# Performance work log

Hardware: AMD Instinct MI355X
Metric: run time of the kernel (lower is better)

## Reference

```python
import jax, jax.numpy as jnp
import numpy as np


def setup_inputs() -> dict:
    key = jax.random.key(0)
    k1, k2 = jax.random.split(key)
    B, D, H, W = 16, 256, 32, 32
    K = 2048
    z = jax.random.normal(k1, (B, D, H, W), dtype=jnp.float32)
    # EmbeddingEMA init: uniform(-1/K, 1/K); plain randn scaled works as a stand-in param
    codebook = jax.random.uniform(k2, (K, D), dtype=jnp.float32,
                                  minval=-1.0 / K, maxval=1.0 / K)
    return {"z": z, "codebook": codebook}


def reference(z, codebook):
    # z: (B, D, H, W) -> (B, H, W, D) -> (n, D)   [normalize == 'none' path]
    B, D, H, W = z.shape
    z_flat = jnp.transpose(z, (0, 2, 3, 1)).reshape(-1, D)          # (n, D)
    z_norm = z_flat
    codebook_norm = codebook                                         # (K, D)

    # squared L2 distance: ||z||^2 + ||c||^2 - 2 z c^T   -> (n, K)
    distance = (jnp.sum(z_norm * z_norm, axis=1, keepdims=True)
                + jnp.sum(codebook_norm * codebook_norm, axis=1)
                - 2.0 * jnp.matmul(z_norm, codebook_norm.T))

    vq_indices = jnp.argmin(distance, axis=1)                        # (n,)
    z_q = codebook_norm[vq_indices]                                  # gather (n, D)

    # straight-through estimator (standard VQ forward output)
    z_q_st = z_norm + jax.lax.stop_gradient(z_q - z_norm)
    out = z_q_st.reshape(B, H, W, D).transpose(0, 3, 1, 2)           # (B, D, H, W)
    return out
```

## Files before the change

kernel.cpp:

```cpp
#include <hip/hip_runtime.h>
#include <stdint.h>


#define D_    256
#define K_    2048
#define HW_   1024
#define MT    64
#define NT    256
#define KT    16
#define SPLIT 4
#define KS    (K_ / SPLIT)
#define CST   256
#define BUFSZ (KT * MT + KT * CST)
#define NPH   ((KS / NT) * KT)
#define NPIX  16384

typedef float v2f __attribute__((ext_vector_type(2)));

__device__ __forceinline__ void gload16(const float* g, float* l) {
    auto* gp = reinterpret_cast<const __attribute__((address_space(1))) uint32_t*>(
        reinterpret_cast<uintptr_t>(g));
    auto* lp = reinterpret_cast<__attribute__((address_space(3))) uint32_t*>(
        reinterpret_cast<uintptr_t>(l));
    __builtin_amdgcn_global_load_lds(gp, lp, 16, 0, 0);
}

__device__ __forceinline__ float pw8(const float r[8]) {
    float t01 = __fadd_rn(r[0], r[1]);
    float t23 = __fadd_rn(r[2], r[3]);
    float L   = __fadd_rn(t01, t23);
    float t45 = __fadd_rn(r[4], r[5]);
    float t67 = __fadd_rn(r[6], r[7]);
    float R   = __fadd_rn(t45, t67);
    return __fadd_rn(L, R);
}

__global__ __launch_bounds__(256) void prep_k(const float* __restrict__ z,
                                              const float* __restrict__ cb,
                                              float* __restrict__ ct,
                                              float* __restrict__ An,
                                              float* __restrict__ Bn) {
    __shared__ float t[64][65];
    int tid = threadIdx.x;
    int bx  = blockIdx.x;
    if (bx < 128) {
        int k0 = (bx & 31) << 6;
        int d0 = (bx >> 5) << 6;
        #pragma unroll
        for (int it = 0; it < 4; ++it) {
            int u  = (it << 8) + tid;
            int kk = u >> 4;
            int dd = (u & 15) << 2;
            float4 v = *reinterpret_cast<const float4*>(
                cb + (size_t)(k0 + kk) * D_ + d0 + dd);
            t[kk][dd + 0] = v.x; t[kk][dd + 1] = v.y;
            t[kk][dd + 2] = v.z; t[kk][dd + 3] = v.w;
        }
        __syncthreads();
        #pragma unroll
        for (int it = 0; it < 4; ++it) {
            int u  = (it << 8) + tid;
            int dd = u >> 4;
            int kk = (u & 15) << 2;
            float4 o;
            o.x = t[kk + 0][dd]; o.y = t[kk + 1][dd];
            o.z = t[kk + 2][dd]; o.w = t[kk + 3][dd];
            *reinterpret_cast<float4*>(ct + (size_t)(d0 + dd) * K_ + k0 + kk) = o;
        }
    } else if (bx < 136) {
        int row = (bx - 128) * 256 + tid;
        const float4* p = reinterpret_cast<const float4*>(cb + (size_t)row * D_);
        float rA[8], rB[8];
        #pragma unroll
        for (int j = 0; j < 8; ++j) { rA[j] = 0.f; rB[j] = 0.f; }
        #pragma unroll
        for (int q = 0; q < 64; ++q) {
            float4 v = p[q];
            float pv[4] = {__fmul_rn(v.x, v.x), __fmul_rn(v.y, v.y),
                           __fmul_rn(v.z, v.z), __fmul_rn(v.w, v.w)};
            if (q < 32) {
                #pragma unroll
                for (int l = 0; l < 4; ++l)
                    rA[(4 * q + l) & 7] = __fadd_rn(rA[(4 * q + l) & 7], pv[l]);
            } else {
                #pragma unroll
                for (int l = 0; l < 4; ++l)
                    rB[(4 * q + l) & 7] = __fadd_rn(rB[(4 * q + l) & 7], pv[l]);
            }
        }
        Bn[row] = __fadd_rn(pw8(rA), pw8(rB));
    } else {
        int blk = bx - 136;
        int b   = blk >> 2;
        int hw0 = (blk & 3) << 8;
        const float* zb = z + (size_t)b * (D_ * HW_) + hw0 + tid;
        float rA[8], rB[8];
        #pragma unroll
        for (int j = 0; j < 8; ++j) { rA[j] = 0.f; rB[j] = 0.f; }
        #pragma unroll 8
        for (int d = 0; d < 128; ++d) {
            float v = zb[(size_t)d * HW_];
            rA[d & 7] = __fadd_rn(rA[d & 7], __fmul_rn(v, v));
        }
        #pragma unroll 8
        for (int d = 128; d < 256; ++d) {
            float v = zb[(size_t)d * HW_];
            rB[d & 7] = __fadd_rn(rB[d & 7], __fmul_rn(v, v));
        }
        An[(size_t)b * HW_ + hw0 + tid] = __fadd_rn(pw8(rA), pw8(rB));
    }
}

__global__ __launch_bounds__(256, 2) void vq_k(const float* __restrict__ z,
                                               const float* __restrict__ ct,
                                               const float* __restrict__ An,
                                               const float* __restrict__ Bn,
                                               float* __restrict__ pscore,
                                               int* __restrict__ pidx) {
    __shared__ float smem[2 * BUFSZ];
    float* rs = smem;
    int*   ri = (int*)(smem + MT * 33);

    const int tid  = threadIdx.x;
    const int lane = tid & 63;
    const int w    = tid >> 6;
    const int tn   = (tid & 7) | (w << 3);
    const int tm   = (tid >> 3) & 7;
    const int blk  = blockIdx.x;
    const int p    = blk / SPLIT;
    const int s    = blk % SPLIT;
    const int b      = p >> 4;
    const int hwbase = (p & 15) << 6;
    const float* zbase = z + (size_t)b * (D_ * HW_) + hwbase;
    const float* ctS   = ct + s * KS;

    const float* zsrc = zbase + (size_t)((w << 2) + (lane >> 4)) * HW_
                              + ((lane & 15) << 2);

    float bs[8]; int bi[8];
    #pragma unroll
    for (int i = 0; i < 8; ++i) { bs[i] = 1e30f; bi[i] = 0; }
    v2f acc[8][4];
    #pragma unroll
    for (int i = 0; i < 8; ++i)
        #pragma unroll
        for (int jp = 0; jp < 4; ++jp) acc[i][jp] = (v2f){0.f, 0.f};

    #define STAGE(ph)                                                         \
        do {                                                                  \
            int buf_ = (ph) & 1, kc_ = (ph) & 15, nc_ = (ph) >> 4;            \
            float* zb_ = smem + buf_ * BUFSZ;                                 \
            float* cb_ = zb_ + KT * MT;                                       \
            gload16(zsrc + (size_t)kc_ * (KT * HW_), zb_ + (w << 2) * MT);    \
            _Pragma("unroll")                                                 \
            for (int r = 0; r < 4; ++r) {                                     \
                int row = (w << 2) + r;                                       \
                gload16(ctS + (size_t)((kc_ << 4) + row) * K_ + nc_ * NT      \
                            + (lane << 2),                                    \
                        cb_ + row * CST);                                     \
            }                                                                 \
        } while (0)

    STAGE(0);

    for (int ph = 0; ph < NPH; ++ph) {
        __syncthreads();
        if (ph < NPH - 1) STAGE(ph + 1);
        const float* zb_ = smem + (ph & 1) * BUFSZ;
        const float* cb_ = zb_ + KT * MT;
        #pragma unroll
        for (int d = 0; d < KT; ++d) {
            const float* zr = zb_ + d * MT + (tm << 3);
            float4 a0 = *reinterpret_cast<const float4*>(zr);
            float4 a1 = *reinterpret_cast<const float4*>(zr + 4);
            const float* cr = cb_ + d * CST + (tn << 3);
            float4 b0 = *reinterpret_cast<const float4*>(cr);
            float4 b1 = *reinterpret_cast<const float4*>(cr + 4);
            v2f bp0 = {b0.x, b0.y}, bp1 = {b0.z, b0.w};
            v2f bp2 = {b1.x, b1.y}, bp3 = {b1.z, b1.w};
            float az[8] = {a0.x, a0.y, a0.z, a0.w, a1.x, a1.y, a1.z, a1.w};
            #pragma unroll
            for (int i = 0; i < 8; ++i) {
                v2f ai = {az[i], az[i]};
                acc[i][0] = __builtin_elementwise_fma(ai, bp0, acc[i][0]);
                acc[i][1] = __builtin_elementwise_fma(ai, bp1, acc[i][1]);
                acc[i][2] = __builtin_elementwise_fma(ai, bp2, acc[i][2]);
                acc[i][3] = __builtin_elementwise_fma(ai, bp3, acc[i][3]);
            }
        }
        if ((ph & 15) == 15) {
            int nc = ph >> 4;
            #pragma unroll
            for (int j = 0; j < 8; ++j) {
                int ng = s * KS + nc * NT + (tn << 3) + j;
                float bn = Bn[ng];
                #pragma unroll
                for (int i = 0; i < 8; ++i) {
                    float an = An[(size_t)b * HW_ + hwbase + (tm << 3) + i];
                    float sc = __fsub_rn(__fadd_rn(an, bn),
                                         __fmul_rn(2.0f, acc[i][j >> 1][j & 1]));
                    if (sc < bs[i]) { bs[i] = sc; bi[i] = ng; }
                }
            }
            #pragma unroll
            for (int i = 0; i < 8; ++i) {
                acc[i][0] = (v2f){0.f, 0.f}; acc[i][1] = (v2f){0.f, 0.f};
                acc[i][2] = (v2f){0.f, 0.f}; acc[i][3] = (v2f){0.f, 0.f};
            }
        }
    }
    #undef STAGE

    __syncthreads();
    #pragma unroll
    for (int i = 0; i < 8; ++i) {
        int m = (tm << 3) + i;
        rs[m * 33 + tn] = bs[i];
        ri[m * 33 + tn] = bi[i];
    }
    __syncthreads();
    if (tid < MT) {
        int   m    = tid;
        float best = rs[m * 33];
        int   bidx = ri[m * 33];
        for (int t = 1; t < 32; ++t) {
            float sv = rs[m * 33 + t];
            int   ix = ri[m * 33 + t];
            if (sv < best || (sv == best && ix < bidx)) { best = sv; bidx = ix; }
        }
        int g = b * HW_ + hwbase + m;
        pscore[s * NPIX + g] = best;
        pidx[s * NPIX + g]   = bidx;
    }
}

__global__ __launch_bounds__(256) void fin_k(const float* __restrict__ cb,
                                             const float* __restrict__ pscore,
                                             const int* __restrict__ pidx,
                                             float* __restrict__ out) {
    __shared__ int idxs[MT];
    int tid = threadIdx.x;
    int p   = blockIdx.x;
    int b      = p >> 4;
    int hwbase = (p & 15) << 6;
    if (tid < MT) {
        int g = b * HW_ + hwbase + tid;
        float best = pscore[g];
        int   bidx = pidx[g];
        #pragma unroll
        for (int s = 1; s < SPLIT; ++s) {
            float sv = pscore[s * NPIX + g];
            int   ix = pidx[s * NPIX + g];
            if (sv < best || (sv == best && ix < bidx)) { best = sv; bidx = ix; }
        }
        idxs[tid] = bidx;
    }
    __syncthreads();
    float* obase = out + (size_t)b * (D_ * HW_) + hwbase;
    #pragma unroll
    for (int it = 0; it < 16; ++it) {
        int u  = (it << 8) + tid;
        int dd = u >> 4;
        int m4 = u & 15;
        int i0 = idxs[(m4 << 2) + 0];
        int i1 = idxs[(m4 << 2) + 1];
        int i2 = idxs[(m4 << 2) + 2];
        int i3 = idxs[(m4 << 2) + 3];
        float4 o;
        o.x = cb[(size_t)i0 * D_ + dd];
        o.y = cb[(size_t)i1 * D_ + dd];
        o.z = cb[(size_t)i2 * D_ + dd];
        o.w = cb[(size_t)i3 * D_ + dd];
        *reinterpret_cast<float4*>(obase + (size_t)dd * HW_ + (m4 << 2)) = o;
    }
}

extern "C" void kernel_launch(void* const* d_in, const int* in_sizes, int n_in,
                              void* d_out, int out_size, void* d_ws, size_t ws_size,
                              hipStream_t stream) {
    const float* z  = (const float*)d_in[0];
    const float* cb = (const float*)d_in[1];
    float* pscore = (float*)d_ws;
    int*   pidx   = (int*)(pscore + SPLIT * NPIX);
    float* An     = (float*)(pidx + SPLIT * NPIX);
    float* Bn     = An + NPIX;
    float* ct     = Bn + K_;
    float* out    = (float*)d_out;

    prep_k<<<dim3(200), dim3(256), 0, stream>>>(z, cb, ct, An, Bn);
    vq_k<<<dim3(256 * SPLIT), dim3(256), 0, stream>>>(z, ct, An, Bn, pscore, pidx);
    fin_k<<<dim3(256), dim3(256), 0, stream>>>(cb, pscore, pidx, out);
}
```

Measured before the change: 295.3 us.

## Widen codebook tile to cover the full split with 8x16 register accumulators

Result: faster. 281.3 us (-4.7%).

```diff
diff --git a/kernel.cpp b/kernel.cpp
--- a/kernel.cpp
+++ b/kernel.cpp
@@ -6,13 +6,12 @@
 #define K_    2048
 #define HW_   1024
 #define MT    64
-#define NT    256
 #define KT    16
 #define SPLIT 4
 #define KS    (K_ / SPLIT)
-#define CST   256
+#define CST   512
 #define BUFSZ (KT * MT + KT * CST)
-#define NPH   ((KS / NT) * KT)
+#define NPH   (D_ / KT)
 #define NPIX  16384
 
 typedef float v2f __attribute__((ext_vector_type(2)));
@@ -140,24 +139,25 @@
     float bs[8]; int bi[8];
     #pragma unroll
     for (int i = 0; i < 8; ++i) { bs[i] = 1e30f; bi[i] = 0; }
-    v2f acc[8][4];
+    v2f acc[8][8];
     #pragma unroll
     for (int i = 0; i < 8; ++i)
         #pragma unroll
-        for (int jp = 0; jp < 4; ++jp) acc[i][jp] = (v2f){0.f, 0.f};
+        for (int q = 0; q < 8; ++q) acc[i][q] = (v2f){0.f, 0.f};
 
     #define STAGE(ph)                                                         \
         do {                                                                  \
-            int buf_ = (ph) & 1, kc_ = (ph) & 15, nc_ = (ph) >> 4;            \
+            int buf_ = (ph) & 1, kc_ = (ph);                                  \
             float* zb_ = smem + buf_ * BUFSZ;                                 \
             float* cb_ = zb_ + KT * MT;                                       \
             gload16(zsrc + (size_t)kc_ * (KT * HW_), zb_ + (w << 2) * MT);    \
             _Pragma("unroll")                                                 \
             for (int r = 0; r < 4; ++r) {                                     \
                 int row = (w << 2) + r;                                       \
-                gload16(ctS + (size_t)((kc_ << 4) + row) * K_ + nc_ * NT      \
-                            + (lane << 2),                                    \
-                        cb_ + row * CST);                                     \
+                const float* src_ = ctS + (size_t)((kc_ << 4) + row) * K_     \
+                                        + (lane << 2);                        \
+                gload16(src_,       cb_ + row * CST);                         \
+                gload16(src_ + 256, cb_ + row * CST + 256);                   \
             }                                                                 \
         } while (0)
 
@@ -176,8 +176,12 @@
             const float* cr = cb_ + d * CST + (tn << 3);
             float4 b0 = *reinterpret_cast<const float4*>(cr);
             float4 b1 = *reinterpret_cast<const float4*>(cr + 4);
+            float4 b2 = *reinterpret_cast<const float4*>(cr + 256);
+            float4 b3 = *reinterpret_cast<const float4*>(cr + 260);
             v2f bp0 = {b0.x, b0.y}, bp1 = {b0.z, b0.w};
             v2f bp2 = {b1.x, b1.y}, bp3 = {b1.z, b1.w};
+            v2f bp4 = {b2.x, b2.y}, bp5 = {b2.z, b2.w};
+            v2f bp6 = {b3.x, b3.y}, bp7 = {b3.z, b3.w};
             float az[8] = {a0.x, a0.y, a0.z, a0.w, a1.x, a1.y, a1.z, a1.w};
             #pragma unroll
             for (int i = 0; i < 8; ++i) {
@@ -186,30 +190,31 @@
                 acc[i][1] = __builtin_elementwise_fma(ai, bp1, acc[i][1]);
                 acc[i][2] = __builtin_elementwise_fma(ai, bp2, acc[i][2]);
                 acc[i][3] = __builtin_elementwise_fma(ai, bp3, acc[i][3]);
+                acc[i][4] = __builtin_elementwise_fma(ai, bp4, acc[i][4]);
+                acc[i][5] = __builtin_elementwise_fma(ai, bp5, acc[i][5]);
+                acc[i][6] = __builtin_elementwise_fma(ai, bp6, acc[i][6]);
+                acc[i][7] = __builtin_elementwise_fma(ai, bp7, acc[i][7]);
             }
         }
-        if ((ph & 15) == 15) {
-            int nc = ph >> 4;
-            #pragma unroll
-            for (int j = 0; j < 8; ++j) {
-                int ng = s * KS + nc * NT + (tn << 3) + j;
-                float bn = Bn[ng];
-                #pragma unroll
-                for (int i = 0; i < 8; ++i) {
-                    float an = An[(size_t)b * HW_ + hwbase + (tm << 3) + i];
-                    float sc = __fsub_rn(__fadd_rn(an, bn),
-                                         __fmul_rn(2.0f, acc[i][j >> 1][j & 1]));
-                    if (sc < bs[i]) { bs[i] = sc; bi[i] = ng; }
-                }
-            }
+    }
+    #undef STAGE
+
+    #pragma unroll
+    for (int h = 0; h < 2; ++h) {
+        #pragma unroll
+        for (int jj = 0; jj < 8; ++jj) {
+            int q  = (h << 2) + (jj >> 1);
+            int ng = s * KS + h * 256 + (tn << 3) + jj;
+            float bn = Bn[ng];
             #pragma unroll
             for (int i = 0; i < 8; ++i) {
-                acc[i][0] = (v2f){0.f, 0.f}; acc[i][1] = (v2f){0.f, 0.f};
-                acc[i][2] = (v2f){0.f, 0.f}; acc[i][3] = (v2f){0.f, 0.f};
+                float an = An[(size_t)b * HW_ + hwbase + (tm << 3) + i];
+                float sc = __fsub_rn(__fadd_rn(an, bn),
+                                     __fmul_rn(2.0f, acc[i][q][jj & 1]));
+                if (sc < bs[i]) { bs[i] = sc; bi[i] = ng; }
             }
         }
     }
-    #undef STAGE
 
     __syncthreads();
     #pragma unroll
```
